# Kernel optimization log

Hardware: AMD Instinct MI355X
Metric: run time of the kernel (lower is better)

Reference implementation:

```python
import jax, jax.numpy as jnp
import numpy as np

D_MODEL = 1024
NUM_HEADS = 16
D_K = D_MODEL // NUM_HEADS
WINDOW = 256


def setup_inputs() -> dict:
    key = jax.random.key(0)
    ks = jax.random.split(key, 11)
    B, S, D = 2, 2048, D_MODEL
    scale = 1.0 / np.sqrt(D)
    inp = {
        "q": jax.random.normal(ks[0], (B, S, D), jnp.float32),
        "k": jax.random.normal(ks[1], (B, S, D), jnp.float32),
        "v": jax.random.normal(ks[2], (B, S, D), jnp.float32),
        "Wq": jax.random.normal(ks[3], (D, D), jnp.float32) * scale,
        "bq": jnp.zeros((D,), jnp.float32),
        "Wk": jax.random.normal(ks[4], (D, D), jnp.float32) * scale,
        "bk": jnp.zeros((D,), jnp.float32),
        "Wv": jax.random.normal(ks[5], (D, D), jnp.float32) * scale,
        "bv": jnp.zeros((D,), jnp.float32),
        "Wo": jax.random.normal(ks[6], (D, D), jnp.float32) * scale,
        "bo": jnp.zeros((D,), jnp.float32),
    }
    return inp


def _split_heads(x):
    B, S, _ = x.shape
    return x.reshape(B, S, NUM_HEADS, D_K).transpose(0, 2, 1, 3)  # [B,H,S,d_k]


def reference(q, k, v, Wq, bq, Wk, bk, Wv, bv, Wo, bo):
    B, S, D = q.shape
    qh = _split_heads(q @ Wq + bq)
    kh = _split_heads(k @ Wk + bk)
    vh = _split_heads(v @ Wv + bv)

    # dense scores then sliding-window band mask (|i-j| <= WINDOW), as in SparseAttention
    scores = jnp.einsum("bhqd,bhkd->bhqk", qh, kh) / jnp.sqrt(jnp.float32(D_K))
    idx = jnp.arange(S)
    band = jnp.abs(idx[:, None] - idx[None, :]) <= WINDOW  # [S,S]
    scores = jnp.where(band[None, None], scores, -jnp.inf)
    attn = jax.nn.softmax(scores, axis=-1)

    out = jnp.einsum("bhqk,bhkd->bhqd", attn, vh)
    out = out.transpose(0, 2, 1, 3).reshape(B, S, D)  # combine heads
    out = out @ Wo + bo
    return out, attn
```

## Files before the change

kernel.cpp:

```cpp
#include <hip/hip_runtime.h>


constexpr int Bb = 2, Ss = 2048, Dd = 1024, Hh = 16, WINw = 256;
constexpr size_t XS_SLAB = (size_t)4096 * 2048;
constexpr size_t WT_SLAB = (size_t)1024 * 2048;
constexpr size_t QB_SLAB = (size_t)4096 * 1024;

typedef short s16x8 __attribute__((ext_vector_type(8)));
typedef float f32x4 __attribute__((ext_vector_type(4)));

typedef __attribute__((address_space(3))) unsigned int lds_uint;
typedef const __attribute__((address_space(1))) unsigned int gbl_uint;

__device__ __forceinline__ void gld_lds16(const void* g, void* l) {
  __builtin_amdgcn_global_load_lds((gbl_uint*)g, (lds_uint*)l, 16, 0, 0);
}

__device__ __forceinline__ void lgkm_barrier() {
  asm volatile("s_waitcnt lgkmcnt(0)" ::: "memory");
  __builtin_amdgcn_s_barrier();
}

__device__ inline unsigned short f2bf(float x) {
  unsigned u = __float_as_uint(x);
  u += 0x7fff + ((u >> 16) & 1);
  return (unsigned short)(u >> 16);
}
__device__ inline float bf2f(unsigned short h) {
  return __uint_as_float(((unsigned)h) << 16);
}

__global__ __launch_bounds__(256) void convert_xw(
    const float* __restrict__ x0, const float* __restrict__ x1,
    const float* __restrict__ x2, unsigned short* __restrict__ Xs,
    const float* __restrict__ w0, const float* __restrict__ w1,
    const float* __restrict__ w2, const float* __restrict__ w3,
    unsigned short* __restrict__ Wt) {
  __shared__ float T[64][65];
  const int id = blockIdx.x;
  const int t = threadIdx.x;
  if (id < 12288) {
    int z = id >> 12;
    int bx = id & 4095;
    const float* src = z == 0 ? x0 : (z == 1 ? x1 : x2);
    unsigned short* dst = Xs + (size_t)z * XS_SLAB;
    size_t idx = ((size_t)bx * 256 + t) * 4;
    int r = (int)(idx >> 10);
    int c = (int)(idx & 1023);
    f32x4 v = *(const f32x4*)&src[idx];
    unsigned short hi[4], lo[4];
#pragma unroll
    for (int i = 0; i < 4; ++i) {
      float vi = v[i];
      hi[i] = f2bf(vi);
      lo[i] = f2bf(vi - bf2f(hi[i]));
    }
    ushort4 h4 = {hi[0], hi[1], hi[2], hi[3]};
    ushort4 l4 = {lo[0], lo[1], lo[2], lo[3]};
    *(ushort4*)&dst[(size_t)r * 2048 + c] = h4;
    *(ushort4*)&dst[(size_t)r * 2048 + 1024 + c] = l4;
  } else {
    int wid = id - 12288;
    int z = wid >> 8;
    int by = (wid >> 4) & 15;
    int bx = wid & 15;
    const float* W = z == 0 ? w0 : (z == 1 ? w1 : (z == 2 ? w2 : w3));
    unsigned short* dst = Wt + (size_t)z * WT_SLAB;
    int k0 = by * 64, n0 = bx * 64;
#pragma unroll
    for (int i = 0; i < 4; ++i) {
      int row = (t >> 4) + i * 16;
      int c4 = (t & 15) * 4;
      f32x4 v = *(const f32x4*)&W[(size_t)(k0 + row) * 1024 + n0 + c4];
      T[row][c4 + 0] = v[0]; T[row][c4 + 1] = v[1];
      T[row][c4 + 2] = v[2]; T[row][c4 + 3] = v[3];
    }
    __syncthreads();
    int n = t >> 2;
    int kc = (t & 3) * 16;
    unsigned short hi[16], lo[16];
#pragma unroll
    for (int j = 0; j < 16; ++j) {
      float x = T[kc + j][n];
      hi[j] = f2bf(x);
      lo[j] = f2bf(x - bf2f(hi[j]));
    }
    size_t base = (size_t)(n0 + n) * 2048 + k0 + kc;
#pragma unroll
    for (int j4 = 0; j4 < 4; ++j4) {
      ushort4 h4 = {hi[j4 * 4], hi[j4 * 4 + 1], hi[j4 * 4 + 2], hi[j4 * 4 + 3]};
      ushort4 l4 = {lo[j4 * 4], lo[j4 * 4 + 1], lo[j4 * 4 + 2], lo[j4 * 4 + 3]};
      *(ushort4*)&dst[base + j4 * 4] = h4;
      *(ushort4*)&dst[base + 1024 + j4 * 4] = l4;
    }
  }
}

__global__ __launch_bounds__(256, 3) void gemm_qkv(
    const unsigned short* __restrict__ Abase,
    const unsigned short* __restrict__ Wtbase,
    unsigned short* __restrict__ Cbase, const float* __restrict__ bb0,
    const float* __restrict__ bb1, const float* __restrict__ bb2) {
  __shared__ s16x8 As[2][512];
  __shared__ s16x8 Bs[2][512];
  int z = blockIdx.z;
  const unsigned short* A = Abase + (size_t)z * XS_SLAB;
  const unsigned short* Wt = Wtbase + (size_t)z * WT_SLAB;
  const float* bias = z == 0 ? bb0 : (z == 1 ? bb1 : bb2);
  const float scl = (z == 0) ? 0.125f : 1.0f;

  const int t = threadIdx.x;
  const int lane = t & 63, wave = t >> 6;
  const int wm = wave & 1, wn = wave >> 1;
  const int bm = blockIdx.y * 128, bn = blockIdx.x * 128;

  f32x4 acc[4][4] = {};

  const int s0 = t, s1 = t + 256;
  const int r0 = s0 >> 2, c0 = (s0 & 3) ^ ((r0 >> 1) & 3);
  const int r1 = s1 >> 2, c1 = (s1 & 3) ^ ((r1 >> 1) & 3);
  const unsigned short* A0 = A + (size_t)(bm + r0) * 2048 + c0 * 8;
  const unsigned short* A1 = A + (size_t)(bm + r1) * 2048 + c1 * 8;
  const unsigned short* B0 = Wt + (size_t)(bn + r0) * 2048 + c0 * 8;
  const unsigned short* B1 = Wt + (size_t)(bn + r1) * 2048 + c1 * 8;

  const int m15 = lane & 15, q = lane >> 4;

  gld_lds16(A0, &As[0][wave * 64]);
  gld_lds16(A1, &As[0][256 + wave * 64]);
  gld_lds16(B0, &Bs[0][wave * 64]);
  gld_lds16(B1, &Bs[0][256 + wave * 64]);
  __syncthreads();

  int cur = 0;
  for (int kb = 0; kb < 3072; kb += 32) {
    const int kn = kb + 32;
    if (kn < 3072) {
      int asrc = kn < 1024 ? kn : kn - 1024;
      int wsrc = kn < 2048 ? kn : kn - 2048;
      gld_lds16(A0 + asrc, &As[cur ^ 1][wave * 64]);
      gld_lds16(A1 + asrc, &As[cur ^ 1][256 + wave * 64]);
      gld_lds16(B0 + wsrc, &Bs[cur ^ 1][wave * 64]);
      gld_lds16(B1 + wsrc, &Bs[cur ^ 1][256 + wave * 64]);
    }

    s16x8 af[4], bf[4];
#pragma unroll
    for (int mt = 0; mt < 4; ++mt) {
      int r = wm * 64 + mt * 16 + m15;
      af[mt] = As[cur][r * 4 + (q ^ ((r >> 1) & 3))];
    }
#pragma unroll
    for (int nt = 0; nt < 4; ++nt) {
      int r = wn * 64 + nt * 16 + m15;
      bf[nt] = Bs[cur][r * 4 + (q ^ ((r >> 1) & 3))];
    }
#pragma unroll
    for (int mt = 0; mt < 4; ++mt)
#pragma unroll
      for (int nt = 0; nt < 4; ++nt)
        acc[mt][nt] = __builtin_amdgcn_mfma_f32_16x16x32_bf16(
            af[mt], bf[nt], acc[mt][nt], 0, 0, 0);

    if (kn < 3072) {
      __syncthreads();
      cur ^= 1;
    }
  }

#pragma unroll
  for (int nt = 0; nt < 4; ++nt) {
    int col = bn + wn * 64 + nt * 16 + m15;
    float bv = bias[col];
#pragma unroll
    for (int mt = 0; mt < 4; ++mt) {
      int rowb = bm + wm * 64 + mt * 16 + q * 4;
#pragma unroll
      for (int i = 0; i < 4; ++i) {
        float val = (acc[mt][nt][i] + bv) * scl;
        (Cbase + (size_t)z * QB_SLAB)[(size_t)(rowb + i) * 1024 + col] =
            f2bf(val);
      }
    }
  }
}

__global__ __launch_bounds__(256, 2) void gemm_out(
    const unsigned short* __restrict__ A,
    const unsigned short* __restrict__ Wt,
    float* __restrict__ C, const float* __restrict__ bias) {
  __shared__ s16x8 As[2][256];
  __shared__ s16x8 Bs[2][512];
  const int t = threadIdx.x;
  const int lane = t & 63, wave = t >> 6;
  const int wm = wave & 1, wn = wave >> 1;
  const int bm = blockIdx.y * 64, bn = blockIdx.x * 128;

  f32x4 acc[2][4] = {};

  const int ra = t >> 2, ca = (t & 3) ^ ((ra >> 1) & 3);
  const int s0 = t, s1 = t + 256;
  const int r0 = s0 >> 2, c0 = (s0 & 3) ^ ((r0 >> 1) & 3);
  const int r1 = s1 >> 2, c1 = (s1 & 3) ^ ((r1 >> 1) & 3);
  const unsigned short* Ap = A + (size_t)(bm + ra) * 2048 + ca * 8;
  const unsigned short* B0 = Wt + (size_t)(bn + r0) * 2048 + c0 * 8;
  const unsigned short* B1 = Wt + (size_t)(bn + r1) * 2048 + c1 * 8;

  const int m15 = lane & 15, q = lane >> 4;

  gld_lds16(Ap, &As[0][wave * 64]);
  gld_lds16(B0, &Bs[0][wave * 64]);
  gld_lds16(B1, &Bs[0][256 + wave * 64]);
  __syncthreads();

  int cur = 0;
  for (int kb = 0; kb < 3072; kb += 32) {
    const int kn = kb + 32;
    if (kn < 3072) {
      int asrc = kn < 1024 ? kn : kn - 1024;
      int wsrc = kn < 2048 ? kn : kn - 2048;
      gld_lds16(Ap + asrc, &As[cur ^ 1][wave * 64]);
      gld_lds16(B0 + wsrc, &Bs[cur ^ 1][wave * 64]);
      gld_lds16(B1 + wsrc, &Bs[cur ^ 1][256 + wave * 64]);
    }

    s16x8 af[2], bf[4];
#pragma unroll
    for (int mt = 0; mt < 2; ++mt) {
      int r = wm * 32 + mt * 16 + m15;
      af[mt] = As[cur][r * 4 + (q ^ ((r >> 1) & 3))];
    }
#pragma unroll
    for (int nt = 0; nt < 4; ++nt) {
      int r = wn * 64 + nt * 16 + m15;
      bf[nt] = Bs[cur][r * 4 + (q ^ ((r >> 1) & 3))];
    }
#pragma unroll
    for (int mt = 0; mt < 2; ++mt)
#pragma unroll
      for (int nt = 0; nt < 4; ++nt)
        acc[mt][nt] = __builtin_amdgcn_mfma_f32_16x16x32_bf16(
            af[mt], bf[nt], acc[mt][nt], 0, 0, 0);

    if (kn < 3072) {
      __syncthreads();
      cur ^= 1;
    }
  }

#pragma unroll
  for (int nt = 0; nt < 4; ++nt) {
    int col = bn + wn * 64 + nt * 16 + m15;
    float bv = bias[col];
#pragma unroll
    for (int mt = 0; mt < 2; ++mt) {
      int rowb = bm + wm * 32 + mt * 16 + q * 4;
#pragma unroll
      for (int i = 0; i < 4; ++i) {
        __builtin_nontemporal_store(
            acc[mt][nt][i] + bv, &C[(size_t)(rowb + i) * 1024 + col]);
      }
    }
  }
}

__global__ __launch_bounds__(256) void transpose_v(
    const unsigned short* __restrict__ Vb, unsigned short* __restrict__ Vt) {
  __shared__ unsigned short T[64][88];
  const int b = blockIdx.z, h = blockIdx.y, s0 = blockIdx.x * 64;
  const int t = threadIdx.x;
  {
    int row = t >> 2, part = t & 3;
    const unsigned short* src =
        Vb + (size_t)(b * Ss + s0 + row) * 1024 + h * 64 + part * 16;
    s16x8 v0 = *(const s16x8*)src;
    s16x8 v1 = *(const s16x8*)(src + 8);
    *(s16x8*)&T[row][part * 16] = v0;
    *(s16x8*)&T[row][part * 16 + 8] = v1;
  }
  __syncthreads();
  {
    int d = t & 63, sw = t >> 6;
    unsigned short tmp[16];
#pragma unroll
    for (int i = 0; i < 16; ++i) tmp[i] = T[sw * 16 + i][d];
    unsigned short* dst =
        Vt + ((size_t)((b * Hh + h) * 64 + d)) * 2048 + s0 + sw * 16;
    *(s16x8*)dst = *(const s16x8*)&tmp[0];
    *(s16x8*)(dst + 8) = *(const s16x8*)&tmp[8];
  }
}

constexpr int SW3 = 556;
__global__ __launch_bounds__(256) void attn_v4(
    const unsigned short* __restrict__ Qb, const unsigned short* __restrict__ Kb,
    const unsigned short* __restrict__ Vt, float* __restrict__ attn,
    unsigned short* __restrict__ XsAO) {
  __shared__ float P[16 * SW3];
  const int t = threadIdx.x;
  const int lane = t & 63, wave = t >> 6;
  const int m15 = lane & 15, quad = lane >> 4;
  const int bid = blockIdx.x;
  const int qt = bid & 127, h = (bid >> 7) & 15, b = bid >> 11;
  const int q0 = qt * 16;
  int jlo = q0 - WINw; if (jlo < 0) jlo = 0;
  int jhi = q0 + 15 + WINw; if (jhi > Ss - 1) jhi = Ss - 1;
  const int ncols = jhi - jlo + 1;
  const int ntiles = ncols >> 4;

  {
    const unsigned short* qrow =
        Qb + (size_t)(b * Ss + q0 + m15) * 1024 + h * 64 + quad * 8;
    s16x8 aq0 = *(const s16x8*)qrow;
    s16x8 aq1 = *(const s16x8*)(qrow + 32);
    for (int nt = wave; nt < ntiles; nt += 4) {
      const unsigned short* krow =
          Kb + (size_t)(b * Ss + jlo + nt * 16 + m15) * 1024 + h * 64 + quad * 8;
      s16x8 b0 = *(const s16x8*)krow;
      s16x8 b1 = *(const s16x8*)(krow + 32);
      f32x4 c = {0.f, 0.f, 0.f, 0.f};
      __builtin_amdgcn_s_setprio(1);
      c = __builtin_amdgcn_mfma_f32_16x16x32_bf16(aq0, b0, c, 0, 0, 0);
      c = __builtin_amdgcn_mfma_f32_16x16x32_bf16(aq1, b1, c, 0, 0, 0);
      __builtin_amdgcn_s_setprio(0);
      float* pp = &P[(quad * 4) * SW3 + nt * 16 + m15];
#pragma unroll
      for (int i = 0; i < 4; ++i) pp[i * SW3] = c[i];
    }
  }
  lgkm_barrier();

  {
#pragma unroll
    for (int ri = 0; ri < 4; ++ri) {
      const int r = wave * 4 + ri;
      const int qq = q0 + r;
      int lo = qq - WINw; if (lo < 0) lo = 0;
      int hi = qq + WINw; if (hi > Ss - 1) hi = Ss - 1;
      const int clo = lo - jlo, chi = hi - jlo;
      float sv[9];
      bool ib[9];
      float m = -1e30f;
#pragma unroll
      for (int k2 = 0; k2 < 9; ++k2) {
        int c = k2 * 64 + lane;
        bool inb = (c >= clo) && (c <= chi);
        ib[k2] = inb;
        float vv = inb ? P[r * SW3 + c] : -1e30f;
        sv[k2] = vv;
        m = fmaxf(m, vv);
      }
#pragma unroll
      for (int off = 32; off; off >>= 1) m = fmaxf(m, __shfl_xor(m, off, 64));
      float e[9], l = 0.f;
#pragma unroll
      for (int k2 = 0; k2 < 9; ++k2) { e[k2] = __expf(sv[k2] - m); l += e[k2]; }
#pragma unroll
      for (int off = 32; off; off >>= 1) l += __shfl_xor(l, off, 64);
      const float inv = 1.f / l;
#pragma unroll
      for (int k2 = 0; k2 < 9; ++k2) {
        int c = k2 * 64 + lane;
        if (c < 544) P[r * SW3 + c] = ib[k2] ? e[k2] * inv : 0.f;
      }
      float* arow = attn + ((size_t)((b * Hh + h) * Ss + qq)) * Ss;
#pragma unroll
      for (int i = 0; i < 8; ++i) {
        int col = i * 256 + lane * 4;
        int c = col - jlo;
        f32x4 v = {0.f, 0.f, 0.f, 0.f};
        if (c >= 0 && c <= 540) v = *(const f32x4*)&P[r * SW3 + c];
        __builtin_nontemporal_store(v, (f32x4*)&arow[col]);
      }
    }
  }
  lgkm_barrier();

  {
    const int ntk = (ncols + 31) >> 5;
    const unsigned short* vtrow =
        Vt + ((size_t)((b * Hh + h) * 64 + wave * 16 + m15)) * 2048 + jlo +
        quad * 8;
    f32x4 o = {0.f, 0.f, 0.f, 0.f};
    for (int ks = 0; ks < ntk; ++ks) {
      const float* pa = &P[m15 * SW3 + ks * 32 + quad * 8];
      f32x4 p0 = *(const f32x4*)pa;
      f32x4 p1 = *(const f32x4*)(pa + 4);
      s16x8 af;
#pragma unroll
      for (int i = 0; i < 4; ++i) af[i] = (short)f2bf(p0[i]);
#pragma unroll
      for (int i = 0; i < 4; ++i) af[4 + i] = (short)f2bf(p1[i]);
      s16x8 bf = *(const s16x8*)(vtrow + ks * 32);
      __builtin_amdgcn_s_setprio(1);
      o = __builtin_amdgcn_mfma_f32_16x16x32_bf16(af, bf, o, 0, 0, 0);
      __builtin_amdgcn_s_setprio(0);
    }
    const int dcol = h * 64 + wave * 16 + m15;
#pragma unroll
    for (int i = 0; i < 4; ++i) {
      int row = q0 + quad * 4 + i;
      unsigned short hi = f2bf(o[i]);
      unsigned short lo = f2bf(o[i] - bf2f(hi));
      unsigned short* dst = XsAO + (size_t)(b * Ss + row) * 2048 + dcol;
      dst[0] = hi;
      dst[1024] = lo;
    }
  }
}

extern "C" void kernel_launch(void* const* d_in, const int* in_sizes, int n_in,
                              void* d_out, int out_size, void* d_ws,
                              size_t ws_size, hipStream_t stream) {
  const float* q  = (const float*)d_in[0];
  const float* k  = (const float*)d_in[1];
  const float* v  = (const float*)d_in[2];
  const float* Wq = (const float*)d_in[3];
  const float* bq = (const float*)d_in[4];
  const float* Wk = (const float*)d_in[5];
  const float* bk = (const float*)d_in[6];
  const float* Wv = (const float*)d_in[7];
  const float* bv = (const float*)d_in[8];
  const float* Wo = (const float*)d_in[9];
  const float* bo = (const float*)d_in[10];

  float* out = (float*)d_out;
  float* attn = out + (size_t)Bb * Ss * Dd;

  unsigned short* Xs   = (unsigned short*)d_ws;
  unsigned short* XsAO = Xs + 3 * XS_SLAB;
  unsigned short* Wt   = XsAO + XS_SLAB;
  unsigned short* Qb   = Wt + 4 * WT_SLAB;
  unsigned short* Kb   = Qb + QB_SLAB;
  unsigned short* Vb   = Kb + QB_SLAB;
  unsigned short* Vt   = Vb + QB_SLAB;

  hipLaunchKernelGGL(convert_xw, dim3(12288 + 1024), dim3(256), 0, stream,
                     q, k, v, Xs, Wq, Wk, Wv, Wo, Wt);
  hipLaunchKernelGGL(gemm_qkv, dim3(8, 32, 3), dim3(256), 0, stream,
                     Xs, Wt, Qb, bq, bk, bv);
  hipLaunchKernelGGL(transpose_v, dim3(32, 16, 2), dim3(256), 0, stream,
                     Vb, Vt);
  hipLaunchKernelGGL(attn_v4, dim3(Bb * Hh * (Ss / 16)), dim3(256), 0, stream,
                     Qb, Kb, Vt, attn, XsAO);
  hipLaunchKernelGGL(gemm_out, dim3(8, 64, 1), dim3(256), 0, stream,
                     XsAO, Wt + 3 * WT_SLAB, out, bo);
}
```

Baseline: 784.1 us.

## Zero-fill attention matrix inside QKV GEMM and write only band in attention

The QKV GEMM now zero-fills the full dense attention-probability output with nontemporal stores interleaved into its K loop, so the 512MB write overlaps MFMA compute. The attention kernel then writes only the in-band columns instead of full 2048-wide rows. Both GEMMs also remap block indices with a swizzle, changing tile traversal order for cache reuse. The risk is that the extra stores contend with GEMM loads for memory bandwidth, and correctness now depends on the GEMM running before the attention kernel.

```diff
diff --git a/kernel.cpp b/kernel.cpp
--- a/kernel.cpp
+++ b/kernel.cpp
@@ -5,6 +5,7 @@
 constexpr size_t XS_SLAB = (size_t)4096 * 2048;
 constexpr size_t WT_SLAB = (size_t)1024 * 2048;
 constexpr size_t QB_SLAB = (size_t)4096 * 1024;
+constexpr size_t ATTN_BYTES = (size_t)Bb * Hh * Ss * Ss * 4;
 
 typedef short s16x8 __attribute__((ext_vector_type(8)));
 typedef float f32x4 __attribute__((ext_vector_type(4)));
@@ -100,7 +101,8 @@
     const unsigned short* __restrict__ Abase,
     const unsigned short* __restrict__ Wtbase,
     unsigned short* __restrict__ Cbase, const float* __restrict__ bb0,
-    const float* __restrict__ bb1, const float* __restrict__ bb2) {
+    const float* __restrict__ bb1, const float* __restrict__ bb2,
+    float* __restrict__ attnz) {
   __shared__ s16x8 As[2][512];
   __shared__ s16x8 Bs[2][512];
   int z = blockIdx.z;
@@ -112,7 +114,15 @@
   const int t = threadIdx.x;
   const int lane = t & 63, wave = t >> 6;
   const int wm = wave & 1, wn = wave >> 1;
-  const int bm = blockIdx.y * 128, bn = blockIdx.x * 128;
+
+  const int flat = blockIdx.x + (blockIdx.y << 3);
+  const int swz = (flat & 7) * 32 + (flat >> 3);
+  const int bm = (swz >> 3) * 128, bn = (swz & 7) * 128;
+
+  const int flat3 = flat + (z << 8);
+  const size_t zbase = (size_t)(flat3 * 4 + wave) * 196608;
+  char* const az = (char*)attnz;
+  const f32x4 zv = {0.f, 0.f, 0.f, 0.f};
 
   f32x4 acc[4][4] = {};
 
@@ -144,6 +154,13 @@
       gld_lds16(B1 + wsrc, &Bs[cur ^ 1][256 + wave * 64]);
     }
 
+    {
+      size_t off = zbase + (size_t)(kb >> 5) * 2048 + (size_t)(lane << 4);
+      if (off < ATTN_BYTES) __builtin_nontemporal_store(zv, (f32x4*)(az + off));
+      off += 1024;
+      if (off < ATTN_BYTES) __builtin_nontemporal_store(zv, (f32x4*)(az + off));
+    }
+
     s16x8 af[4], bf[4];
 #pragma unroll
     for (int mt = 0; mt < 4; ++mt) {
@@ -194,7 +211,10 @@
   const int t = threadIdx.x;
   const int lane = t & 63, wave = t >> 6;
   const int wm = wave & 1, wn = wave >> 1;
-  const int bm = blockIdx.y * 64, bn = blockIdx.x * 128;
+
+  const int flat = blockIdx.x + (blockIdx.y << 3);
+  const int swz = (flat & 7) * 64 + (flat >> 3);
+  const int bm = (swz >> 3) * 64, bn = (swz & 7) * 128;
 
   f32x4 acc[2][4] = {};
 
@@ -292,7 +312,7 @@
 }
 
 constexpr int SW3 = 556;
-__global__ __launch_bounds__(256) void attn_v4(
+__global__ __launch_bounds__(256) void attn_v5(
     const unsigned short* __restrict__ Qb, const unsigned short* __restrict__ Kb,
     const unsigned short* __restrict__ Vt, float* __restrict__ attn,
     unsigned short* __restrict__ XsAO) {
@@ -363,14 +383,14 @@
         int c = k2 * 64 + lane;
         if (c < 544) P[r * SW3 + c] = ib[k2] ? e[k2] * inv : 0.f;
       }
-      float* arow = attn + ((size_t)((b * Hh + h) * Ss + qq)) * Ss;
-#pragma unroll
-      for (int i = 0; i < 8; ++i) {
-        int col = i * 256 + lane * 4;
-        int c = col - jlo;
-        f32x4 v = {0.f, 0.f, 0.f, 0.f};
-        if (c >= 0 && c <= 540) v = *(const f32x4*)&P[r * SW3 + c];
-        __builtin_nontemporal_store(v, (f32x4*)&arow[col]);
+      float* arow = attn + ((size_t)((b * Hh + h) * Ss + qq)) * Ss + jlo;
+#pragma unroll
+      for (int i = 0; i < 3; ++i) {
+        int c = i * 256 + lane * 4;
+        if (c < ncols) {
+          f32x4 v = *(const f32x4*)&P[r * SW3 + c];
+          __builtin_nontemporal_store(v, (f32x4*)&arow[c]);
+        }
       }
     }
   }
@@ -438,10 +458,10 @@
   hipLaunchKernelGGL(convert_xw, dim3(12288 + 1024), dim3(256), 0, stream,
                      q, k, v, Xs, Wq, Wk, Wv, Wo, Wt);
   hipLaunchKernelGGL(gemm_qkv, dim3(8, 32, 3), dim3(256), 0, stream,
-                     Xs, Wt, Qb, bq, bk, bv);
+                     Xs, Wt, Qb, bq, bk, bv, attn);
   hipLaunchKernelGGL(transpose_v, dim3(32, 16, 2), dim3(256), 0, stream,
                      Vb, Vt);
-  hipLaunchKernelGGL(attn_v4, dim3(Bb * Hh * (Ss / 16)), dim3(256), 0, stream,
+  hipLaunchKernelGGL(attn_v5, dim3(Bb * Hh * (Ss / 16)), dim3(256), 0, stream,
                      Qb, Kb, Vt, attn, XsAO);
   hipLaunchKernelGGL(gemm_out, dim3(8, 64, 1), dim3(256), 0, stream,
                      XsAO, Wt + 3 * WT_SLAB, out, bo);
```

After: 779.3 us. Within noise of the previous version (-0.6%).
